# Performance work log

Measured on AMD Instinct MI355X. Metric: run time of the kernel, lower is better.

The kernel has to match this reference:

```python
import jax, jax.numpy as jnp
import numpy as np
import math
from jax import lax


def quick_gelu(v):
    return v * jax.nn.sigmoid(1.702 * v)


def setup_inputs() -> dict:
    key = jax.random.key(0)
    k0, k1, k2, k3 = jax.random.split(key, 4)
    B, N, C, dim = 64, 1024, 768, 8
    x = jax.random.normal(k0, (B, N, C), dtype=jnp.float32)
    # adapter_down: Linear(C -> dim), xavier-ish init
    Wd = jax.random.normal(k1, (C, dim), dtype=jnp.float32) * (1.0 / math.sqrt(C))
    bd = jnp.zeros((dim,), dtype=jnp.float32)
    # adapter_conv: Conv2d(dim, dim, 3, stride=1, pad=1), HWIO layout
    Wc = jax.random.normal(k2, (3, 3, dim, dim), dtype=jnp.float32) * (1.0 / math.sqrt(9 * dim))
    bc = jnp.zeros((dim,), dtype=jnp.float32)
    # adapter_up: Linear(dim -> C); torch inits this to zeros, but use small
    # random values so the output/gradients are non-trivial for testing.
    Wu = jax.random.normal(k3, (dim, C), dtype=jnp.float32) * 0.02
    bu = jnp.zeros((C,), dtype=jnp.float32)
    return {"x": x, "Wd": Wd, "bd": bd, "Wc": Wc, "bc": bc, "Wu": Wu, "bu": bu}


def reference(x, Wd, bd, Wc, bc, Wu, bu):
    B, N, C = x.shape
    H = int(math.isqrt(N))  # N is a static perfect square (patch grid)
    dim = Wd.shape[1]
    # down projection: [B, N, C] -> [B, N, dim]
    x_down = jnp.einsum("bnc,cd->bnd", x, Wd) + bd
    # reshape to NHWC patch grid, activate, 3x3 same-pad conv
    x_patch = quick_gelu(x_down.reshape(B, H, H, dim))
    x_patch = lax.conv_general_dilated(
        x_patch, Wc, window_strides=(1, 1), padding="SAME",
        dimension_numbers=("NHWC", "HWIO", "NHWC")) + bc
    # flatten back, activate (dropout = identity in eval), up projection
    x_down = quick_gelu(x_patch.reshape(B, N, dim))
    x_up = jnp.einsum("bnd,dc->bnc", x_down, Wu) + bu
    return x_up
```

## Files before the change

kernel.cpp:

```cpp
#include <hip/hip_runtime.h>

#define B_  64
#define N_  1024
#define H_  32
#define C_  768
#define D_  8

__device__ __forceinline__ float qgelu(float v) {
    return v / (1.0f + __expf(-1.702f * v));
}

__device__ __forceinline__ void reduce8(float* acc, int lane) {
    {
        const bool hi = lane & 1;
#pragma unroll
        for (int j = 0; j < 4; ++j) {
            const float a = acc[j], b = acc[j + 4];
            acc[j] = hi ? b : a;
            acc[j + 4] = hi ? a : b;
        }
#pragma unroll
        for (int j = 0; j < 4; ++j)
            acc[j] += __shfl_xor(acc[j + 4], 1, 64);
    }
    {
        const bool hi = lane & 2;
#pragma unroll
        for (int j = 0; j < 2; ++j) {
            const float a = acc[j], b = acc[j + 2];
            acc[j] = hi ? b : a;
            acc[j + 2] = hi ? a : b;
        }
#pragma unroll
        for (int j = 0; j < 2; ++j)
            acc[j] += __shfl_xor(acc[j + 2], 2, 64);
    }
    {
        const bool hi = lane & 4;
        const float a = acc[0], b = acc[1];
        acc[0] = hi ? b : a;
        acc[1] = hi ? a : b;
        acc[0] += __shfl_xor(acc[1], 4, 64);
    }
    acc[0] += __shfl_xor(acc[0], 8, 64);
    acc[0] += __shfl_xor(acc[0], 16, 64);
    acc[0] += __shfl_xor(acc[0], 32, 64);
}

__global__ __launch_bounds__(256, 3) void k_down(
    const float* __restrict__ x, const float* __restrict__ Wd,
    const float* __restrict__ bd, float* __restrict__ t1, int nrows)
{
    __shared__ float sW[D_ * C_];
    for (int i = threadIdx.x; i < D_ * C_; i += 256) {
        int d = i / C_, c = i - d * C_;
        sW[i] = Wd[c * D_ + d];
    }
    __syncthreads();

    const int wid  = threadIdx.x >> 6;
    const int lane = threadIdx.x & 63;

    float4 w[3][D_];
#pragma unroll
    for (int k = 0; k < 3; ++k)
#pragma unroll
        for (int d = 0; d < D_; ++d)
            w[k][d] = *(const float4*)&sW[d * C_ + (lane + k * 64) * 4];

    const int dl = 4 * (lane & 1) + 2 * ((lane >> 1) & 1) + ((lane >> 2) & 1);
    const float bias = bd[dl];

    const int npairs = nrows >> 1;
    const int stride = gridDim.x * 4;
    for (int p = blockIdx.x * 4 + wid; p < npairs; p += stride) {
        const int r0 = p * 2;
        const float4* x0 = (const float4*)(x + (size_t)r0 * C_);
        const float4* x1 = x0 + (C_ / 4);

        float4 v0[3], v1[3];
#pragma unroll
        for (int k = 0; k < 3; ++k) {
            v0[k] = x0[lane + k * 64];
            v1[k] = x1[lane + k * 64];
        }

        float a0[D_], a1[D_];
#pragma unroll
        for (int d = 0; d < D_; ++d) { a0[d] = 0.0f; a1[d] = 0.0f; }

#pragma unroll
        for (int k = 0; k < 3; ++k) {
#pragma unroll
            for (int d = 0; d < D_; ++d) {
                a0[d] += v0[k].x * w[k][d].x + v0[k].y * w[k][d].y
                       + v0[k].z * w[k][d].z + v0[k].w * w[k][d].w;
                a1[d] += v1[k].x * w[k][d].x + v1[k].y * w[k][d].y
                       + v1[k].z * w[k][d].z + v1[k].w * w[k][d].w;
            }
        }

        reduce8(a0, lane);
        reduce8(a1, lane);

        if (lane < 16) {
            const float s = (lane & 8) ? a1[0] : a0[0];
            const int   r = r0 + ((lane >> 3) & 1);
            t1[(size_t)r * D_ + dl] = qgelu(s + bias);
        }
    }
}

__global__ __launch_bounds__(256, 4) void k_conv(
    const float* __restrict__ t1, const float* __restrict__ Wc,
    const float* __restrict__ bc, float* __restrict__ t2)
{
    __shared__ float sIn[10 * H_ * D_];
    __shared__ float sWc[9 * D_ * D_];
    __shared__ float sbc[D_];

    const int img   = blockIdx.x >> 2;
    const int strip = blockIdx.x & 3;
    const int h0    = strip * 8;
    const float* in = t1 + (size_t)img * N_ * D_;

#pragma unroll
    for (int j = 0; j < 10; ++j) {
        const int i  = threadIdx.x + j * 256;
        const int lr = i >> 8;
        const int rem = i & 255;
        const int g  = h0 - 1 + lr;
        sIn[i] = (g >= 0 && g < H_) ? in[(size_t)g * H_ * D_ + rem] : 0.0f;
    }
    for (int i = threadIdx.x; i < 9 * D_ * D_; i += 256) sWc[i] = Wc[i];
    if (threadIdx.x < D_) sbc[threadIdx.x] = bc[threadIdx.x];
    __syncthreads();

    const int lh = threadIdx.x >> 5;
    const int w  = threadIdx.x & 31;
    float acc[D_];
#pragma unroll
    for (int co = 0; co < D_; ++co) acc[co] = sbc[co];

#pragma unroll
    for (int kh = 0; kh < 3; ++kh) {
        const int lrow = lh + kh;
#pragma unroll
        for (int kw = 0; kw < 3; ++kw) {
            const int ww = w + kw - 1;
            if (ww < 0 || ww >= H_) continue;
            const float* ip = &sIn[(lrow * H_ + ww) * D_];
            const float* wp = &sWc[(kh * 3 + kw) * D_ * D_];
#pragma unroll
            for (int ci = 0; ci < D_; ++ci) {
                const float iv = ip[ci];
#pragma unroll
                for (int co = 0; co < D_; ++co)
                    acc[co] += iv * wp[ci * D_ + co];
            }
        }
    }
    float4 o0, o1;
    o0.x = qgelu(acc[0]); o0.y = qgelu(acc[1]);
    o0.z = qgelu(acc[2]); o0.w = qgelu(acc[3]);
    o1.x = qgelu(acc[4]); o1.y = qgelu(acc[5]);
    o1.z = qgelu(acc[6]); o1.w = qgelu(acc[7]);
    float* tp = t2 + ((size_t)img * N_ + (size_t)(h0 + lh) * H_ + w) * D_;
    *(float4*)tp       = o0;
    *(float4*)(tp + 4) = o1;
}

__global__ __launch_bounds__(256, 3) void k_up(
    const float* __restrict__ t2, const float* __restrict__ Wu,
    const float* __restrict__ bu, float* __restrict__ out, int nrows)
{
    const int wid  = threadIdx.x >> 6;
    const int lane = threadIdx.x & 63;

    float4 w[3][D_];
    float4 bias[3];
#pragma unroll
    for (int j = 0; j < 3; ++j) {
        bias[j] = *(const float4*)&bu[(lane + j * 64) * 4];
#pragma unroll
        for (int d = 0; d < D_; ++d)
            w[j][d] = *(const float4*)&Wu[d * C_ + (lane + j * 64) * 4];
    }

    const int stride = gridDim.x * 4;
    for (int row = blockIdx.x * 4 + wid; row < nrows; row += stride) {
        const float4* rp = (const float4*)(t2 + (size_t)row * D_);
        const float4 ra = rp[0];
        const float4 rb = rp[1];
        const float rv[D_] = { ra.x, ra.y, ra.z, ra.w, rb.x, rb.y, rb.z, rb.w };

#pragma unroll
        for (int j = 0; j < 3; ++j) {
            float4 o = bias[j];
#pragma unroll
            for (int d = 0; d < D_; ++d) {
                o.x += rv[d] * w[j][d].x;
                o.y += rv[d] * w[j][d].y;
                o.z += rv[d] * w[j][d].z;
                o.w += rv[d] * w[j][d].w;
            }
            *(float4*)&out[(size_t)row * C_ + (size_t)(lane + j * 64) * 4] = o;
        }
    }
}

extern "C" void kernel_launch(void* const* d_in, const int* in_sizes, int n_in,
                              void* d_out, int out_size, void* d_ws, size_t ws_size,
                              hipStream_t stream) {
    const float* x  = (const float*)d_in[0];
    const float* Wd = (const float*)d_in[1];
    const float* bd = (const float*)d_in[2];
    const float* Wc = (const float*)d_in[3];
    const float* bc = (const float*)d_in[4];
    const float* Wu = (const float*)d_in[5];
    const float* bu = (const float*)d_in[6];
    float* out = (float*)d_out;

    const int nrows = B_ * N_;
    float* t1 = (float*)d_ws;
    float* t2 = t1 + (size_t)nrows * D_;

    k_down<<<768, 256, 0, stream>>>(x, Wd, bd, t1, nrows);
    k_conv<<<B_ * 4, 256, 0, stream>>>(t1, Wc, bc, t2);
    k_up<<<768, 256, 0, stream>>>(t2, Wu, bu, out, nrows);
}
```

Baseline: 118.5 us.

## Stage down-projection input rows into double-buffered LDS via async global-to-LDS loads

The down-projection kernel now gives each block a fixed span of 128 rows. It streams them eight at a time into a double-buffered LDS area using global_load_lds, instead of loading x straight into registers in a grid-stride loop. The goal is to overlap fetching the next tile with the dot products on the current one. Shared memory use doubles, so occupancy drops to 2 blocks per CU and the grid shrinks to 512 blocks. The barriers around each stage may drain outstanding loads, which could limit the intended overlap.

```diff
diff --git a/kernel.cpp b/kernel.cpp
--- a/kernel.cpp
+++ b/kernel.cpp
@@ -8,6 +8,12 @@
 
 __device__ __forceinline__ float qgelu(float v) {
     return v / (1.0f + __expf(-1.702f * v));
+}
+
+__device__ __forceinline__ void async_cp16(const float* gp, float* lp) {
+    __builtin_amdgcn_global_load_lds(
+        (const __attribute__((address_space(1))) void*)gp,
+        (__attribute__((address_space(3))) void*)lp, 16, 0, 0);
 }
 
 __device__ __forceinline__ void reduce8(float* acc, int lane) {
@@ -47,68 +53,75 @@
     acc[0] += __shfl_xor(acc[0], 32, 64);
 }
 
-__global__ __launch_bounds__(256, 3) void k_down(
+__global__ __launch_bounds__(256, 2) void k_down(
     const float* __restrict__ x, const float* __restrict__ Wd,
     const float* __restrict__ bd, float* __restrict__ t1, int nrows)
 {
-    __shared__ float sW[D_ * C_];
-    for (int i = threadIdx.x; i < D_ * C_; i += 256) {
-        int d = i / C_, c = i - d * C_;
-        sW[i] = Wd[c * D_ + d];
-    }
-    __syncthreads();
+    __shared__ float buf[2][D_ * C_];
 
     const int wid  = threadIdx.x >> 6;
     const int lane = threadIdx.x & 63;
 
+    for (int i = threadIdx.x; i < D_ * C_; i += 256) {
+        const int c = i >> 3, d = i & 7;
+        buf[0][d * C_ + c] = Wd[i];
+    }
+    __syncthreads();
     float4 w[3][D_];
 #pragma unroll
     for (int k = 0; k < 3; ++k)
 #pragma unroll
         for (int d = 0; d < D_; ++d)
-            w[k][d] = *(const float4*)&sW[d * C_ + (lane + k * 64) * 4];
-
+            w[k][d] = *(const float4*)&buf[0][d * C_ + (k * 64 + lane) * 4];
     const int dl = 4 * (lane & 1) + 2 * ((lane >> 1) & 1) + ((lane >> 2) & 1);
     const float bias = bd[dl];
-
-    const int npairs = nrows >> 1;
-    const int stride = gridDim.x * 4;
-    for (int p = blockIdx.x * 4 + wid; p < npairs; p += stride) {
-        const int r0 = p * 2;
-        const float4* x0 = (const float4*)(x + (size_t)r0 * C_);
-        const float4* x1 = x0 + (C_ / 4);
-
-        float4 v0[3], v1[3];
+    __syncthreads();
+
+    const int row0 = blockIdx.x * 128;
+
+#define STAGE(T, BUF)                                                        \
+    {                                                                        \
+        const float* gp0 = x + (size_t)(row0 + (T) * 8) * C_ + wid * 1536;   \
+        float* lp0 = &buf[BUF][wid * 1536];                                  \
+        _Pragma("unroll")                                                    \
+        for (int j = 0; j < 6; ++j)                                          \
+            async_cp16(gp0 + j * 256 + lane * 4, lp0 + j * 256);             \
+    }
+
+    STAGE(0, 0)
+#pragma unroll 1
+    for (int t = 0; t < 16; ++t) {
+        __syncthreads();
+        if (t + 1 < 16) STAGE(t + 1, (t + 1) & 1)
+
+        const float* rowa = &buf[t & 1][(2 * wid) * C_];
+        const float* rowb = rowa + C_;
+        float a0[D_], a1[D_];
+#pragma unroll
+        for (int d = 0; d < D_; ++d) { a0[d] = 0.f; a1[d] = 0.f; }
 #pragma unroll
         for (int k = 0; k < 3; ++k) {
-            v0[k] = x0[lane + k * 64];
-            v1[k] = x1[lane + k * 64];
-        }
-
-        float a0[D_], a1[D_];
-#pragma unroll
-        for (int d = 0; d < D_; ++d) { a0[d] = 0.0f; a1[d] = 0.0f; }
-
-#pragma unroll
-        for (int k = 0; k < 3; ++k) {
+            const float4 va = *(const float4*)&rowa[(k * 64 + lane) * 4];
+            const float4 vb = *(const float4*)&rowb[(k * 64 + lane) * 4];
 #pragma unroll
             for (int d = 0; d < D_; ++d) {
-                a0[d] += v0[k].x * w[k][d].x + v0[k].y * w[k][d].y
-                       + v0[k].z * w[k][d].z + v0[k].w * w[k][d].w;
-                a1[d] += v1[k].x * w[k][d].x + v1[k].y * w[k][d].y
-                       + v1[k].z * w[k][d].z + v1[k].w * w[k][d].w;
+                a0[d] += va.x * w[k][d].x + va.y * w[k][d].y
+                       + va.z * w[k][d].z + va.w * w[k][d].w;
+                a1[d] += vb.x * w[k][d].x + vb.y * w[k][d].y
+                       + vb.z * w[k][d].z + vb.w * w[k][d].w;
             }
         }
-
         reduce8(a0, lane);
         reduce8(a1, lane);
 
         if (lane < 16) {
             const float s = (lane & 8) ? a1[0] : a0[0];
-            const int   r = r0 + ((lane >> 3) & 1);
+            const int   r = row0 + t * 8 + 2 * wid + ((lane >> 3) & 1);
             t1[(size_t)r * D_ + dl] = qgelu(s + bias);
         }
-    }
+        __syncthreads();
+    }
+#undef STAGE
 }
 
 __global__ __launch_bounds__(256, 4) void k_conv(
@@ -225,7 +238,7 @@
     float* t1 = (float*)d_ws;
     float* t2 = t1 + (size_t)nrows * D_;
 
-    k_down<<<768, 256, 0, stream>>>(x, Wd, bd, t1, nrows);
+    k_down<<<512, 256, 0, stream>>>(x, Wd, bd, t1, nrows);
     k_conv<<<B_ * 4, 256, 0, stream>>>(t1, Wc, bc, t2);
     k_up<<<768, 256, 0, stream>>>(t2, Wu, bu, out, nrows);
 }
```

Result: faster. 108.2 us (-8.7%).
